# Optimization experiments

Hardware: AMD Instinct MI355X
Metric: run time of the kernel (lower is better)

The kernel has to match this reference:

```python
import jax, jax.numpy as jnp
import numpy as np

N = 50000
IN_C, HID, OUT_C = 128, 64, 40


def setup_inputs() -> dict:
    key = jax.random.key(0)
    ks = jax.random.split(key, 10)
    x = jax.random.normal(ks[0], (N, IN_C), dtype=jnp.float32)
    edge_index = jax.random.randint(ks[1], (2, 1600000), 0, N, dtype=jnp.int64)
    edge_attr = jax.random.uniform(ks[2], (1600000,), dtype=jnp.float32)
    def lin(k, fan_in, fan_out):
        bound = 1.0 / np.sqrt(fan_in)
        return jax.random.uniform(k, (fan_in, fan_out), jnp.float32, -bound, bound)
    W1 = lin(ks[3], IN_C, HID); b1 = jnp.zeros((HID,), jnp.float32)
    W2 = lin(ks[4], HID, HID); b2 = jnp.zeros((HID,), jnp.float32)
    W3 = lin(ks[5], HID, OUT_C); b3 = jnp.zeros((OUT_C,), jnp.float32)
    return {"x": x, "edge_index": edge_index, "edge_attr": edge_attr,
            "W1": W1, "b1": b1, "W2": W2, "b2": b2, "W3": W3, "b3": b3}


def _gcn_conv(x, src, dst, norm, W, b):
    # h = x W ; out[i] = sum_{(j->i)} norm_e * h[j] ; + bias
    h = x @ W
    msg = norm[:, None] * h[src]          # [E+N, F_out] gathered messages
    out = jax.ops.segment_sum(msg, dst, num_segments=N)
    return out + b


def reference(x, edge_index, edge_attr, W1, b1, W2, b2, W3, b3):
    # GCN normalization with self-loops (fill_value=1), cached across layers.
    loops = jnp.arange(N, dtype=edge_index.dtype)
    src = jnp.concatenate([edge_index[0], loops])
    dst = jnp.concatenate([edge_index[1], loops])
    w = jnp.concatenate([edge_attr, jnp.ones((N,), edge_attr.dtype)])
    deg = jnp.zeros((N,), x.dtype).at[dst].add(w)
    dinv = jnp.where(deg > 0, jax.lax.rsqrt(deg), 0.0)
    norm = dinv[src] * w * dinv[dst]

    h = jax.nn.relu(_gcn_conv(x, src, dst, norm, W1, b1))   # dropout: eval no-op
    h = jax.nn.relu(_gcn_conv(h, src, dst, norm, W2, b2))
    h = jax.nn.relu(_gcn_conv(h, src, dst, norm, W3, b3))
    return jax.nn.log_softmax(h, axis=-1)
```

## Files before the change

kernel.cpp:

```cpp
#include <hip/hip_runtime.h>
#include <math.h>

#define N_NODES 50000
#define E_EDGES 1600000
#define IN_C    128
#define HID     64
#define OUT_C   40

#define BSH     9
#define BNODES  512
#define NB      98
#define CAP     20480
#define TILE    4096
#define P1T     512
#define NPB     16

typedef unsigned int uint;
typedef unsigned short ushort;

__device__ inline float b2f(ushort h) { return __uint_as_float(((uint)h) << 16); }
__device__ inline ushort f2b(float f) {
    uint u = __float_as_uint(f);
    u += 0x7FFFu + ((u >> 16) & 1u);
    return (ushort)(u >> 16);
}
#define BLO(u) __uint_as_float((u) << 16)
#define BHI(u) __uint_as_float((u) & 0xFFFF0000u)
#define FMA8(A, B, v, ww) do { \
    (A).x += (ww) * BLO((v).x); (A).y += (ww) * BHI((v).x); \
    (A).z += (ww) * BLO((v).y); (A).w += (ww) * BHI((v).y); \
    (B).x += (ww) * BLO((v).z); (B).y += (ww) * BHI((v).z); \
    (B).z += (ww) * BLO((v).w); (B).w += (ww) * BHI((v).w); } while (0)

struct EV { uint4 a, b; float wa, wb; };

template <int FW>
__device__ __forceinline__ void issue_ev(uint dvec, int ebase, int end,
                                         const ushort* __restrict__ g,
                                         int grp, int sub, EV& E) {
    uint d0 = __shfl(dvec, grp);
    uint d1 = __shfl(dvec, 8 + grp);
    E.wa = (ebase + grp     < end) ? b2f((ushort)(d0 >> 16)) : 0.0f;
    E.wb = (ebase + 8 + grp < end) ? b2f((ushort)(d1 >> 16)) : 0.0f;
    E.a = ((const uint4*)(g + (size_t)(d0 & 0xFFFFu) * FW))[sub];
    E.b = ((const uint4*)(g + (size_t)(d1 & 0xFFFFu) * FW))[sub];
}

__global__ __launch_bounds__(P1T) void k_bin(const int* __restrict__ ei,
                                             const float* __restrict__ w,
                                             int* __restrict__ bcursor,
                                             uint2* __restrict__ tmp) {
    __shared__ uint2 stage[TILE];
    __shared__ unsigned char sbuck[TILE];
    __shared__ int hist[NB], startb[NB], cursor[NB], baseg[NB];
    __shared__ int sc[128];
    const int tid = threadIdx.x;
    const int e0  = blockIdx.x * TILE;
    const int n   = min(TILE, E_EDGES - e0);

    for (int i = tid; i < NB; i += P1T) hist[i] = 0;
    __syncthreads();

    for (int i = tid; i < n; i += P1T) {
        int d = ei[E_EDGES + e0 + i];
        atomicAdd(&hist[d >> BSH], 1);
    }
    __syncthreads();

    if (tid < 128) sc[tid] = (tid < NB) ? hist[tid] : 0;
    __syncthreads();
    for (int off = 1; off < 128; off <<= 1) {
        int x = 0;
        if (tid < 128 && tid >= off) x = sc[tid - off];
        __syncthreads();
        if (tid < 128) sc[tid] += x;
        __syncthreads();
    }
    if (tid < NB) {
        int st = sc[tid] - hist[tid];
        startb[tid] = st;
        cursor[tid] = st;
        baseg[tid]  = atomicAdd(&bcursor[tid], hist[tid]);
    }
    __syncthreads();

    for (int i = tid; i < n; i += P1T) {
        int   s  = ei[e0 + i];
        int   d  = ei[E_EDGES + e0 + i];
        float wv = w[e0 + i];
        int   b  = d >> BSH;
        int pos = atomicAdd(&cursor[b], 1);
        stage[pos] = make_uint2(((uint)(d & (BNODES - 1)) << 16) | (uint)s,
                                __float_as_uint(wv));
        sbuck[pos] = (unsigned char)b;
    }
    __syncthreads();

    for (int i = tid; i < n; i += P1T) {
        int b = sbuck[i];
        int gpos = baseg[b] + (i - startb[b]);
        tmp[(size_t)b * CAP + gpos] = stage[i];
    }
}

__global__ __launch_bounds__(BNODES) void k_build(const int* __restrict__ bcursor,
                                                  const uint2* __restrict__ tmp,
                                                  int* __restrict__ rowptr,
                                                  float* __restrict__ dinv,
                                                  uint* __restrict__ csr) {
    __shared__ int   hist[BNODES];
    __shared__ float wsum[BNODES];
    __shared__ int   sc[BNODES];
    __shared__ int   sb[128];
    __shared__ int   s_eb;
    const int tid = threadIdx.x;
    const int b   = blockIdx.x;

    if (tid < 128) sb[tid] = (tid < NB) ? bcursor[tid] : 0;
    hist[tid] = 0; wsum[tid] = 0.0f;
    __syncthreads();
    for (int off = 1; off < 128; off <<= 1) {
        int x = (tid < 128 && tid >= off) ? sb[tid - off] : 0;
        __syncthreads();
        if (tid < 128) sb[tid] += x;
        __syncthreads();
    }
    if (tid == 0) s_eb = sb[b] - bcursor[b];
    __syncthreads();
    const int cnt = bcursor[b];
    const int eb  = s_eb;
    const uint2* tb = tmp + (size_t)b * CAP;

    for (int i = tid; i < cnt; i += BNODES) {
        uint2 u = tb[i];
        int dl = u.x >> 16;
        atomicAdd(&hist[dl], 1);
        atomicAdd(&wsum[dl], __uint_as_float(u.y));
    }
    __syncthreads();

    int own = hist[tid];
    sc[tid] = own;
    __syncthreads();
    for (int off = 1; off < BNODES; off <<= 1) {
        int x = (tid >= off) ? sc[tid - off] : 0;
        __syncthreads();
        sc[tid] += x;
        __syncthreads();
    }
    int excl = sc[tid] - own;
    int node = (b << BSH) + tid;
    if (node < N_NODES) {
        rowptr[node] = eb + excl;
        dinv[node]   = rsqrtf(1.0f + wsum[tid]);
    }
    if (b == 0 && tid == 0) rowptr[N_NODES] = E_EDGES;
    hist[tid] = excl;
    __syncthreads();

    for (int i = tid; i < cnt; i += BNODES) {
        uint2 u = tb[i];
        int dl = u.x >> 16;
        int pos = atomicAdd(&hist[dl], 1);
        csr[eb + pos] = ((uint)f2b(__uint_as_float(u.y)) << 16) | (u.x & 0xFFFFu);
    }
}

__global__ __launch_bounds__(256) void k_gemm1(const float* __restrict__ x,
                                               const float* __restrict__ W,
                                               const float* __restrict__ dinv,
                                               ushort* __restrict__ g) {
    __shared__ float sW[IN_C * HID];
    __shared__ float sx[NPB * IN_C];
    const int tid = threadIdx.x;
    const size_t base = (size_t)blockIdx.x * NPB;

    for (int i = tid; i < (IN_C * HID) / 4; i += 256)
        ((float4*)sW)[i] = ((const float4*)W)[i];
    for (int i = tid; i < (NPB * IN_C) / 4; i += 256)
        ((float4*)sx)[i] = ((const float4*)(x + base * IN_C))[i];
    __syncthreads();

    const int wv = tid >> 6, f = tid & 63;
    for (int nn = 0; nn < 4; ++nn) {
        const int nl = wv * 4 + nn;
        const float* row = &sx[nl * IN_C];
        float acc = 0.0f;
#pragma unroll 8
        for (int k = 0; k < IN_C; k += 4) {
            float4 a = *(const float4*)&row[k];
            acc += a.x * sW[(k + 0) * HID + f] + a.y * sW[(k + 1) * HID + f]
                 + a.z * sW[(k + 2) * HID + f] + a.w * sW[(k + 3) * HID + f];
        }
        const size_t node = base + nl;
        g[node * HID + f] = f2b(dinv[node] * acc);
    }
}

template <int F_OUT>
__global__ __launch_bounds__(256) void k_agg_gemm(const int* __restrict__ rowptr,
                                                  const uint* __restrict__ csr,
                                                  const ushort* __restrict__ g,
                                                  const float* __restrict__ dinv,
                                                  const float* __restrict__ bias,
                                                  const float* __restrict__ W,
                                                  ushort* __restrict__ g_next) {
    __shared__ float sW[HID * F_OUT];
    __shared__ float s_act[4][HID];
    const int tid = threadIdx.x;
    for (int i = tid; i < HID * F_OUT; i += 256) sW[i] = W[i];

    const int wv = tid >> 6, lane = tid & 63;
    const int node  = blockIdx.x * 4 + wv;
    const int grp   = lane >> 3;
    const int sub   = lane & 7;
    const int dslot = lane & 15;
    const int beg = rowptr[node], end = rowptr[node + 1];
    const float dv = dinv[node];

    float4 accA = {0.f, 0.f, 0.f, 0.f}, accB = accA;
    if (grp == 0) {
        uint4 v = ((const uint4*)(g + (size_t)node * HID))[sub];
        accA.x = BLO(v.x); accA.y = BHI(v.x); accA.z = BLO(v.y); accA.w = BHI(v.y);
        accB.x = BLO(v.z); accB.y = BHI(v.z); accB.z = BLO(v.w); accB.w = BHI(v.w);
    }

    if (beg < end) {
        uint dv0 = csr[min(beg      + dslot, E_EDGES - 1)];
        uint dv1 = csr[min(beg + 16 + dslot, E_EDGES - 1)];
        uint dv2 = csr[min(beg + 32 + dslot, E_EDGES - 1)];
        EV E0, E1, En;
        issue_ev<HID>(dv0, beg,      end, g, grp, sub, E0);
        issue_ev<HID>(dv1, beg + 16, end, g, grp, sub, E1);
        for (int e = beg; e < end; e += 16) {
            issue_ev<HID>(dv2, e + 32, end, g, grp, sub, En);
            dv2 = csr[min(e + 48 + dslot, E_EDGES - 1)];
            FMA8(accA, accB, E0.a, E0.wa);
            FMA8(accA, accB, E0.b, E0.wb);
            E0 = E1; E1 = En;
        }
    }
#pragma unroll
    for (int m = 8; m <= 32; m <<= 1) {
        accA.x += __shfl_xor(accA.x, m); accA.y += __shfl_xor(accA.y, m);
        accA.z += __shfl_xor(accA.z, m); accA.w += __shfl_xor(accA.w, m);
        accB.x += __shfl_xor(accB.x, m); accB.y += __shfl_xor(accB.y, m);
        accB.z += __shfl_xor(accB.z, m); accB.w += __shfl_xor(accB.w, m);
    }
    if (grp == 0) {
        float4 bA = ((const float4*)bias)[2 * sub];
        float4 bB = ((const float4*)bias)[2 * sub + 1];
        float4 rA, rB;
        rA.x = fmaxf(dv * accA.x + bA.x, 0.f); rA.y = fmaxf(dv * accA.y + bA.y, 0.f);
        rA.z = fmaxf(dv * accA.z + bA.z, 0.f); rA.w = fmaxf(dv * accA.w + bA.w, 0.f);
        rB.x = fmaxf(dv * accB.x + bB.x, 0.f); rB.y = fmaxf(dv * accB.y + bB.y, 0.f);
        rB.z = fmaxf(dv * accB.z + bB.z, 0.f); rB.w = fmaxf(dv * accB.w + bB.w, 0.f);
        ((float4*)&s_act[wv][0])[2 * sub]     = rA;
        ((float4*)&s_act[wv][0])[2 * sub + 1] = rB;
    }
    __syncthreads();
    if (lane < F_OUT) {
        float dot = 0.0f;
#pragma unroll 4
        for (int k = 0; k < HID; k += 4) {
            float4 a = *(const float4*)&s_act[wv][k];
            dot += a.x * sW[(k + 0) * F_OUT + lane] + a.y * sW[(k + 1) * F_OUT + lane]
                 + a.z * sW[(k + 2) * F_OUT + lane] + a.w * sW[(k + 3) * F_OUT + lane];
        }
        g_next[(size_t)node * F_OUT + lane] = f2b(dinv[node] * dot);
    }
}

__global__ __launch_bounds__(256) void k_final_agg(const int* __restrict__ rowptr,
                                                   const uint* __restrict__ csr,
                                                   const ushort* __restrict__ g,
                                                   const float* __restrict__ dinv,
                                                   const float* __restrict__ bias,
                                                   float* __restrict__ out) {
    const int tid = threadIdx.x;
    const int wv = tid >> 6, lane = tid & 63;
    const int node  = blockIdx.x * 4 + wv;
    const int grp   = lane >> 3;
    const int sub   = lane & 7;
    const int dslot = lane & 15;
    const bool live = sub < (OUT_C / 8);
    const int beg = rowptr[node], end = rowptr[node + 1];
    const float dv = dinv[node];

    float4 accA = {0.f, 0.f, 0.f, 0.f}, accB = accA;
    if (grp == 0 && live) {
        uint4 v = ((const uint4*)(g + (size_t)node * OUT_C))[sub];
        accA.x = BLO(v.x); accA.y = BHI(v.x); accA.z = BLO(v.y); accA.w = BHI(v.y);
        accB.x = BLO(v.z); accB.y = BHI(v.z); accB.z = BLO(v.w); accB.w = BHI(v.w);
    }

    if (beg < end) {
        uint dv0 = csr[min(beg      + dslot, E_EDGES - 1)];
        uint dv1 = csr[min(beg + 16 + dslot, E_EDGES - 1)];
        uint dv2 = csr[min(beg + 32 + dslot, E_EDGES - 1)];
        EV E0, E1, En;
        issue_ev<OUT_C>(dv0, beg,      end, g, grp, sub, E0);
        issue_ev<OUT_C>(dv1, beg + 16, end, g, grp, sub, E1);
        for (int e = beg; e < end; e += 16) {
            issue_ev<OUT_C>(dv2, e + 32, end, g, grp, sub, En);
            dv2 = csr[min(e + 48 + dslot, E_EDGES - 1)];
            FMA8(accA, accB, E0.a, E0.wa);
            FMA8(accA, accB, E0.b, E0.wb);
            E0 = E1; E1 = En;
        }
    }
#pragma unroll
    for (int m = 8; m <= 32; m <<= 1) {
        accA.x += __shfl_xor(accA.x, m); accA.y += __shfl_xor(accA.y, m);
        accA.z += __shfl_xor(accA.z, m); accA.w += __shfl_xor(accA.w, m);
        accB.x += __shfl_xor(accB.x, m); accB.y += __shfl_xor(accB.y, m);
        accB.z += __shfl_xor(accB.z, m); accB.w += __shfl_xor(accB.w, m);
    }

    const bool own = (grp == 0) && live;
    float4 vA = {0.f, 0.f, 0.f, 0.f}, vB = vA;
    if (own) {
        float4 bA = ((const float4*)bias)[2 * sub];
        float4 bB = ((const float4*)bias)[2 * sub + 1];
        vA.x = fmaxf(dv * accA.x + bA.x, 0.f); vA.y = fmaxf(dv * accA.y + bA.y, 0.f);
        vA.z = fmaxf(dv * accA.z + bA.z, 0.f); vA.w = fmaxf(dv * accA.w + bA.w, 0.f);
        vB.x = fmaxf(dv * accB.x + bB.x, 0.f); vB.y = fmaxf(dv * accB.y + bB.y, 0.f);
        vB.z = fmaxf(dv * accB.z + bB.z, 0.f); vB.w = fmaxf(dv * accB.w + bB.w, 0.f);
    }
    float mx = own ? fmaxf(fmaxf(fmaxf(vA.x, vA.y), fmaxf(vA.z, vA.w)),
                           fmaxf(fmaxf(vB.x, vB.y), fmaxf(vB.z, vB.w))) : -INFINITY;
#pragma unroll
    for (int off = 1; off < 8; off <<= 1) mx = fmaxf(mx, __shfl_xor(mx, off));
    float se = own ? (expf(vA.x - mx) + expf(vA.y - mx) + expf(vA.z - mx) + expf(vA.w - mx)
                    + expf(vB.x - mx) + expf(vB.y - mx) + expf(vB.z - mx) + expf(vB.w - mx)) : 0.f;
#pragma unroll
    for (int off = 1; off < 8; off <<= 1) se += __shfl_xor(se, off);
    if (own) {
        float lg = mx + logf(se);
        float4 oA, oB;
        oA.x = vA.x - lg; oA.y = vA.y - lg; oA.z = vA.z - lg; oA.w = vA.w - lg;
        oB.x = vB.x - lg; oB.y = vB.y - lg; oB.z = vB.z - lg; oB.w = vB.w - lg;
        ((float4*)(out + (size_t)node * OUT_C))[2 * sub]     = oA;
        ((float4*)(out + (size_t)node * OUT_C))[2 * sub + 1] = oB;
    }
}

extern "C" void kernel_launch(void* const* d_in, const int* in_sizes, int n_in,
                              void* d_out, int out_size, void* d_ws, size_t ws_size,
                              hipStream_t stream) {
    const float* x  = (const float*)d_in[0];
    const int*   ei = (const int*)d_in[1];
    const float* w  = (const float*)d_in[2];
    const float* W1 = (const float*)d_in[3];
    const float* b1 = (const float*)d_in[4];
    const float* W2 = (const float*)d_in[5];
    const float* b2 = (const float*)d_in[6];
    const float* W3 = (const float*)d_in[7];
    const float* b3 = (const float*)d_in[8];
    float* out = (float*)d_out;

    char* ws = (char*)d_ws;
    size_t off = 0;
    auto carve = [&](size_t bytes) {
        char* p = ws + off;
        off += (bytes + 255) & ~(size_t)255;
        return p;
    };
    int*   bcursor = (int*)carve(NB * sizeof(int));
    int*   rowptr  = (int*)carve((N_NODES + 1) * sizeof(int));
    float* dinv    = (float*)carve(N_NODES * sizeof(float));
    uint*  csr     = (uint*)carve((size_t)E_EDGES * sizeof(uint));
    uint2* tmp     = (uint2*)carve((size_t)NB * CAP * sizeof(uint2));
    ushort* g1 = (ushort*)tmp;
    ushort* g2 = g1 + (size_t)N_NODES * HID;
    ushort* g3 = g1;
    (void)ws_size;

    const int nbBin = (E_EDGES + TILE - 1) / TILE;
    const int nbN4  = N_NODES / 4;
    const int nbG1  = N_NODES / NPB;

    hipMemsetAsync(bcursor, 0, NB * sizeof(int), stream);
    k_bin<<<nbBin, P1T, 0, stream>>>(ei, w, bcursor, tmp);
    k_build<<<NB, BNODES, 0, stream>>>(bcursor, tmp, rowptr, dinv, csr);

    k_gemm1<<<nbG1, 256, 0, stream>>>(x, W1, dinv, g1);
    k_agg_gemm<HID><<<nbN4, 256, 0, stream>>>(rowptr, csr, g1, dinv, b1, W2, g2);
    k_agg_gemm<OUT_C><<<nbN4, 256, 0, stream>>>(rowptr, csr, g2, dinv, b2, W3, g3);
    k_final_agg<<<nbN4, 256, 0, stream>>>(rowptr, csr, g3, dinv, b3, out);
}
```

Before: 247.1 us.

## Pad CSR rows to multiples of 16 with packed row info

k_build now lays out each node's edge list padded to a multiple of 16 entries in a per-bucket region of fixed size, zero-filling the padding. Each node's start offset and block count are packed into one word, replacing rowptr and the global scan over bucket counts. The aggregation kernels drop per-edge bounds checks and min() clamps, and use a simpler two-stage software pipeline over 16-edge blocks. Padding adds wasted gathers on node 0 (weight zero), a slightly larger CSR buffer, and serial zero-fill loops per thread. Prefetch depth drops from two blocks ahead to one.

```diff
diff --git a/kernel.cpp b/kernel.cpp
--- a/kernel.cpp
+++ b/kernel.cpp
@@ -11,6 +11,7 @@
 #define BNODES  512
 #define NB      98
 #define CAP     20480
+#define PBS     28160
 #define TILE    4096
 #define P1T     512
 #define NPB     16
@@ -31,20 +32,6 @@
     (A).z += (ww) * BLO((v).y); (A).w += (ww) * BHI((v).y); \
     (B).x += (ww) * BLO((v).z); (B).y += (ww) * BHI((v).z); \
     (B).z += (ww) * BLO((v).w); (B).w += (ww) * BHI((v).w); } while (0)
-
-struct EV { uint4 a, b; float wa, wb; };
-
-template <int FW>
-__device__ __forceinline__ void issue_ev(uint dvec, int ebase, int end,
-                                         const ushort* __restrict__ g,
-                                         int grp, int sub, EV& E) {
-    uint d0 = __shfl(dvec, grp);
-    uint d1 = __shfl(dvec, 8 + grp);
-    E.wa = (ebase + grp     < end) ? b2f((ushort)(d0 >> 16)) : 0.0f;
-    E.wb = (ebase + 8 + grp < end) ? b2f((ushort)(d1 >> 16)) : 0.0f;
-    E.a = ((const uint4*)(g + (size_t)(d0 & 0xFFFFu) * FW))[sub];
-    E.b = ((const uint4*)(g + (size_t)(d1 & 0xFFFFu) * FW))[sub];
-}
 
 __global__ __launch_bounds__(P1T) void k_bin(const int* __restrict__ ei,
                                              const float* __restrict__ w,
@@ -105,32 +92,20 @@
 
 __global__ __launch_bounds__(BNODES) void k_build(const int* __restrict__ bcursor,
                                                   const uint2* __restrict__ tmp,
-                                                  int* __restrict__ rowptr,
+                                                  uint* __restrict__ rowinfo,
                                                   float* __restrict__ dinv,
                                                   uint* __restrict__ csr) {
     __shared__ int   hist[BNODES];
     __shared__ float wsum[BNODES];
     __shared__ int   sc[BNODES];
-    __shared__ int   sb[128];
-    __shared__ int   s_eb;
+    __shared__ int   cur[BNODES];
     const int tid = threadIdx.x;
     const int b   = blockIdx.x;
-
-    if (tid < 128) sb[tid] = (tid < NB) ? bcursor[tid] : 0;
+    const int cnt = bcursor[b];
+    const uint2* tb = tmp + (size_t)b * CAP;
+
     hist[tid] = 0; wsum[tid] = 0.0f;
     __syncthreads();
-    for (int off = 1; off < 128; off <<= 1) {
-        int x = (tid < 128 && tid >= off) ? sb[tid - off] : 0;
-        __syncthreads();
-        if (tid < 128) sb[tid] += x;
-        __syncthreads();
-    }
-    if (tid == 0) s_eb = sb[b] - bcursor[b];
-    __syncthreads();
-    const int cnt = bcursor[b];
-    const int eb  = s_eb;
-    const uint2* tb = tmp + (size_t)b * CAP;
-
     for (int i = tid; i < cnt; i += BNODES) {
         uint2 u = tb[i];
         int dl = u.x >> 16;
@@ -139,8 +114,9 @@
     }
     __syncthreads();
 
-    int own = hist[tid];
-    sc[tid] = own;
+    const int deg  = hist[tid];
+    const int pdeg = (deg + 15) & ~15;
+    sc[tid] = pdeg;
     __syncthreads();
     for (int off = 1; off < BNODES; off <<= 1) {
         int x = (tid >= off) ? sc[tid - off] : 0;
@@ -148,22 +124,22 @@
         sc[tid] += x;
         __syncthreads();
     }
-    int excl = sc[tid] - own;
-    int node = (b << BSH) + tid;
+    const int base = b * PBS + (sc[tid] - pdeg);
+    const int node = (b << BSH) + tid;
     if (node < N_NODES) {
-        rowptr[node] = eb + excl;
-        dinv[node]   = rsqrtf(1.0f + wsum[tid]);
-    }
-    if (b == 0 && tid == 0) rowptr[N_NODES] = E_EDGES;
-    hist[tid] = excl;
+        rowinfo[node] = ((uint)(pdeg >> 4) << 24) | (uint)base;
+        dinv[node]    = rsqrtf(1.0f + wsum[tid]);
+    }
+    cur[tid] = base;
     __syncthreads();
 
     for (int i = tid; i < cnt; i += BNODES) {
         uint2 u = tb[i];
         int dl = u.x >> 16;
-        int pos = atomicAdd(&hist[dl], 1);
-        csr[eb + pos] = ((uint)f2b(__uint_as_float(u.y)) << 16) | (u.x & 0xFFFFu);
-    }
+        int pos = atomicAdd(&cur[dl], 1);
+        csr[pos] = ((uint)f2b(__uint_as_float(u.y)) << 16) | (u.x & 0xFFFFu);
+    }
+    for (int i = deg; i < pdeg; ++i) csr[base + i] = 0u;
 }
 
 __global__ __launch_bounds__(256) void k_gemm1(const float* __restrict__ x,
@@ -198,7 +174,7 @@
 }
 
 template <int F_OUT>
-__global__ __launch_bounds__(256) void k_agg_gemm(const int* __restrict__ rowptr,
+__global__ __launch_bounds__(256) void k_agg_gemm(const uint* __restrict__ rowinfo,
                                                   const uint* __restrict__ csr,
                                                   const ushort* __restrict__ g,
                                                   const float* __restrict__ dinv,
@@ -215,8 +191,10 @@
     const int grp   = lane >> 3;
     const int sub   = lane & 7;
     const int dslot = lane & 15;
-    const int beg = rowptr[node], end = rowptr[node + 1];
+    const uint ri  = rowinfo[node];
+    const int  n16 = (int)(ri >> 24);
     const float dv = dinv[node];
+    const ushort* gs = g + (size_t)sub * 8;
 
     float4 accA = {0.f, 0.f, 0.f, 0.f}, accB = accA;
     if (grp == 0) {
@@ -225,20 +203,26 @@
         accB.x = BLO(v.z); accB.y = BHI(v.z); accB.z = BLO(v.w); accB.w = BHI(v.w);
     }
 
-    if (beg < end) {
-        uint dv0 = csr[min(beg      + dslot, E_EDGES - 1)];
-        uint dv1 = csr[min(beg + 16 + dslot, E_EDGES - 1)];
-        uint dv2 = csr[min(beg + 32 + dslot, E_EDGES - 1)];
-        EV E0, E1, En;
-        issue_ev<HID>(dv0, beg,      end, g, grp, sub, E0);
-        issue_ev<HID>(dv1, beg + 16, end, g, grp, sub, E1);
-        for (int e = beg; e < end; e += 16) {
-            issue_ev<HID>(dv2, e + 32, end, g, grp, sub, En);
-            dv2 = csr[min(e + 48 + dslot, E_EDGES - 1)];
-            FMA8(accA, accB, E0.a, E0.wa);
-            FMA8(accA, accB, E0.b, E0.wb);
-            E0 = E1; E1 = En;
+    if (n16 > 0) {
+        const uint* rp = csr + (ri & 0xFFFFFFu) + dslot;
+        uint d1 = rp[0];
+        uint sA = __shfl(d1, grp), sB = __shfl(d1, 8 + grp);
+        float wA = BHI(sA), wB = BHI(sB);
+        uint4 A = *(const uint4*)(gs + (size_t)(sA & 0xFFFFu) * HID);
+        uint4 B = *(const uint4*)(gs + (size_t)(sB & 0xFFFFu) * HID);
+        d1 = rp[16];
+        for (int blk = 1; blk < n16; ++blk) {
+            uint d2 = rp[(blk + 1) << 4];
+            uint sA2 = __shfl(d1, grp), sB2 = __shfl(d1, 8 + grp);
+            float wA2 = BHI(sA2), wB2 = BHI(sB2);
+            uint4 A2 = *(const uint4*)(gs + (size_t)(sA2 & 0xFFFFu) * HID);
+            uint4 B2 = *(const uint4*)(gs + (size_t)(sB2 & 0xFFFFu) * HID);
+            FMA8(accA, accB, A, wA);
+            FMA8(accA, accB, B, wB);
+            d1 = d2; A = A2; B = B2; wA = wA2; wB = wB2;
         }
+        FMA8(accA, accB, A, wA);
+        FMA8(accA, accB, B, wB);
     }
 #pragma unroll
     for (int m = 8; m <= 32; m <<= 1) {
@@ -271,7 +255,7 @@
     }
 }
 
-__global__ __launch_bounds__(256) void k_final_agg(const int* __restrict__ rowptr,
+__global__ __launch_bounds__(256) void k_final_agg(const uint* __restrict__ rowinfo,
                                                    const uint* __restrict__ csr,
                                                    const ushort* __restrict__ g,
                                                    const float* __restrict__ dinv,
@@ -284,8 +268,10 @@
     const int sub   = lane & 7;
     const int dslot = lane & 15;
     const bool live = sub < (OUT_C / 8);
-    const int beg = rowptr[node], end = rowptr[node + 1];
+    const uint ri  = rowinfo[node];
+    const int  n16 = (int)(ri >> 24);
     const float dv = dinv[node];
+    const ushort* gs = g + (size_t)sub * 8;
 
     float4 accA = {0.f, 0.f, 0.f, 0.f}, accB = accA;
     if (grp == 0 && live) {
@@ -294,20 +280,26 @@
         accB.x = BLO(v.z); accB.y = BHI(v.z); accB.z = BLO(v.w); accB.w = BHI(v.w);
     }
 
-    if (beg < end) {
-        uint dv0 = csr[min(beg      + dslot, E_EDGES - 1)];
-        uint dv1 = csr[min(beg + 16 + dslot, E_EDGES - 1)];
-        uint dv2 = csr[min(beg + 32 + dslot, E_EDGES - 1)];
-        EV E0, E1, En;
-        issue_ev<OUT_C>(dv0, beg,      end, g, grp, sub, E0);
-        issue_ev<OUT_C>(dv1, beg + 16, end, g, grp, sub, E1);
-        for (int e = beg; e < end; e += 16) {
-            issue_ev<OUT_C>(dv2, e + 32, end, g, grp, sub, En);
-            dv2 = csr[min(e + 48 + dslot, E_EDGES - 1)];
-            FMA8(accA, accB, E0.a, E0.wa);
-            FMA8(accA, accB, E0.b, E0.wb);
-            E0 = E1; E1 = En;
+    if (n16 > 0) {
+        const uint* rp = csr + (ri & 0xFFFFFFu) + dslot;
+        uint d1 = rp[0];
+        uint sA = __shfl(d1, grp), sB = __shfl(d1, 8 + grp);
+        float wA = BHI(sA), wB = BHI(sB);
+        uint4 A = *(const uint4*)(gs + (size_t)(sA & 0xFFFFu) * OUT_C);
+        uint4 B = *(const uint4*)(gs + (size_t)(sB & 0xFFFFu) * OUT_C);
+        d1 = rp[16];
+        for (int blk = 1; blk < n16; ++blk) {
+            uint d2 = rp[(blk + 1) << 4];
+            uint sA2 = __shfl(d1, grp), sB2 = __shfl(d1, 8 + grp);
+            float wA2 = BHI(sA2), wB2 = BHI(sB2);
+            uint4 A2 = *(const uint4*)(gs + (size_t)(sA2 & 0xFFFFu) * OUT_C);
+            uint4 B2 = *(const uint4*)(gs + (size_t)(sB2 & 0xFFFFu) * OUT_C);
+            FMA8(accA, accB, A, wA);
+            FMA8(accA, accB, B, wB);
+            d1 = d2; A = A2; B = B2; wA = wA2; wB = wB2;
         }
+        FMA8(accA, accB, A, wA);
+        FMA8(accA, accB, B, wB);
     }
 #pragma unroll
     for (int m = 8; m <= 32; m <<= 1) {
@@ -367,9 +359,9 @@
         return p;
     };
     int*   bcursor = (int*)carve(NB * sizeof(int));
-    int*   rowptr  = (int*)carve((N_NODES + 1) * sizeof(int));
+    uint*  rowinfo = (uint*)carve(N_NODES * sizeof(uint));
     float* dinv    = (float*)carve(N_NODES * sizeof(float));
-    uint*  csr     = (uint*)carve((size_t)E_EDGES * sizeof(uint));
+    uint*  csr     = (uint*)carve(((size_t)NB * PBS + 64) * sizeof(uint));
     uint2* tmp     = (uint2*)carve((size_t)NB * CAP * sizeof(uint2));
     ushort* g1 = (ushort*)tmp;
     ushort* g2 = g1 + (size_t)N_NODES * HID;
@@ -382,10 +374,10 @@
 
     hipMemsetAsync(bcursor, 0, NB * sizeof(int), stream);
     k_bin<<<nbBin, P1T, 0, stream>>>(ei, w, bcursor, tmp);
-    k_build<<<NB, BNODES, 0, stream>>>(bcursor, tmp, rowptr, dinv, csr);
+    k_build<<<NB, BNODES, 0, stream>>>(bcursor, tmp, rowinfo, dinv, csr);
 
     k_gemm1<<<nbG1, 256, 0, stream>>>(x, W1, dinv, g1);
-    k_agg_gemm<HID><<<nbN4, 256, 0, stream>>>(rowptr, csr, g1, dinv, b1, W2, g2);
-    k_agg_gemm<OUT_C><<<nbN4, 256, 0, stream>>>(rowptr, csr, g2, dinv, b2, W3, g3);
-    k_final_agg<<<nbN4, 256, 0, stream>>>(rowptr, csr, g3, dinv, b3, out);
-}
+    k_agg_gemm<HID><<<nbN4, 256, 0, stream>>>(rowinfo, csr, g1, dinv, b1, W2, g2);
+    k_agg_gemm<OUT_C><<<nbN4, 256, 0, stream>>>(rowinfo, csr, g2, dinv, b2, W3, g3);
+    k_final_agg<<<nbN4, 256, 0, stream>>>(rowinfo, csr, g3, dinv, b3, out);
+}
```

New measurement: 242.6 us. About the same (-1.8%).
